# Kernel optimization log

Hardware: AMD Instinct MI355X
Metric: run time of the kernel (lower is better)

The kernel has to match this reference:

```python
import jax, jax.numpy as jnp
import numpy as np

N_NODES = 50000
N_EDGES = 800000
MUL = 32            # multiplicity of 0e and 1o feature irreps
N_SPECIES = 4       # node_attr = 4x0e one-hot
N_BASIS = 8         # radial basis scalars
N_HID = 8           # invariant_neurons
AVG_NEIGH = 16.0
INV_SQRT3 = 1.0 / np.sqrt(3.0).astype(np.float32)


def setup_inputs() -> dict:
    key = jax.random.key(0)
    ks = jax.random.split(key, 16)
    x = jax.random.normal(ks[0], (N_NODES, MUL * 4), jnp.float32)  # 32x0e + 32x1o
    species = jax.random.randint(ks[1], (N_NODES,), 0, N_SPECIES)
    node_attr = jax.nn.one_hot(species, N_SPECIES, dtype=jnp.float32)
    edge_embedding = jax.random.normal(ks[2], (N_EDGES, N_BASIS), jnp.float32)
    edge_attr = jax.random.normal(ks[3], (N_EDGES, 4), jnp.float32)  # 1x0e + 1x1o
    edge_index = jax.random.randint(ks[4], (2, N_EDGES), 0, N_NODES)
    # learned params
    W_lin1_s = jax.random.normal(ks[5], (MUL, MUL), jnp.float32)
    W_lin1_v = jax.random.normal(ks[6], (MUL, MUL), jnp.float32)
    fc_w1 = jax.random.normal(ks[7], (N_BASIS, N_HID), jnp.float32)
    fc_w2 = jax.random.normal(ks[8], (N_HID, 4 * MUL), jnp.float32)  # tp.weight_numel = 4*MUL
    W_lin2_s = jax.random.normal(ks[9], (2 * MUL, MUL), jnp.float32)  # mid simplify: 64x0e
    W_lin2_v = jax.random.normal(ks[10], (2 * MUL, MUL), jnp.float32)  # 64x1o
    W_sc_s = jax.random.normal(ks[11], (MUL, N_SPECIES, MUL), jnp.float32)
    W_sc_v = jax.random.normal(ks[12], (MUL, N_SPECIES, MUL), jnp.float32)
    return dict(node_features=x, node_attr=node_attr, edge_embedding=edge_embedding,
                edge_attr=edge_attr, edge_index=edge_index,
                W_lin1_s=W_lin1_s, W_lin1_v=W_lin1_v, fc_w1=fc_w1, fc_w2=fc_w2,
                W_lin2_s=W_lin2_s, W_lin2_v=W_lin2_v, W_sc_s=W_sc_s, W_sc_v=W_sc_v)


def _forward(node_features, node_attr, edge_embedding, edge_attr, edge_index,
             W_lin1_s, W_lin1_v, fc_w1, fc_w2, W_lin2_s, W_lin2_v, W_sc_s, W_sc_v):
    n = node_features.shape[0]
    xs = node_features[:, :MUL]                       # [N, 32] scalars (0e)
    xv = node_features[:, MUL:].reshape(n, MUL, 3)    # [N, 32, 3] vectors (1o)

    # self-connection: FullyConnectedTensorProduct(feat, 4x0e -> feat), uvw weights
    sc_norm = 1.0 / np.sqrt(MUL * N_SPECIES).astype(np.float32)
    sc_s = jnp.einsum('nu,nv,uvw->nw', xs, node_attr, W_sc_s) * sc_norm
    sc_v = jnp.einsum('nui,nv,uvw->nwi', xv, node_attr, W_sc_v) * sc_norm

    # linear_1: per-irrep channel mixing, 1/sqrt(fan_in)
    l1n = 1.0 / np.sqrt(MUL).astype(np.float32)
    ys = (xs @ W_lin1_s) * l1n
    yv = jnp.einsum('nui,uw->nwi', xv, W_lin1_v) * l1n

    # radial MLP -> per-edge tensor-product weights (4 paths x MUL)
    h = jax.nn.silu((edge_embedding @ fc_w1) / np.sqrt(N_BASIS).astype(np.float32))
    w = (h @ fc_w2) / np.sqrt(N_HID).astype(np.float32)  # [E, 128]
    w00, w01, w10, w11 = jnp.split(w, 4, axis=1)          # instruction order (0,0),(0,1),(1,0),(1,1)

    src = edge_index[0]
    dst = edge_index[1]
    es = ys[src]                                          # [E, 32]
    ev = yv[src]                                          # [E, 32, 3]
    a0 = edge_attr[:, 0]                                  # [E]    0e
    a1 = edge_attr[:, 1:4]                                # [E, 3] 1o

    # per-edge weighted uvu tensor product paths
    o_s_a = w00 * es * a0[:, None]                                       # 0e x 0e -> 0e
    o_s_b = w11 * jnp.einsum('eui,ei->eu', ev, a1) * INV_SQRT3           # 1o x 1o -> 0e
    o_v_a = (w01 * es)[:, :, None] * a1[:, None, :]                      # 0e x 1o -> 1o
    o_v_b = w10[:, :, None] * ev * a0[:, None, None]                     # 1o x 0e -> 1o

    # scatter-sum to destination nodes
    mid_s = jax.ops.segment_sum(jnp.concatenate([o_s_a, o_s_b], axis=1), dst, num_segments=n)
    mid_v = jax.ops.segment_sum(jnp.concatenate([o_v_a, o_v_b], axis=1), dst, num_segments=n)
    inv = 1.0 / np.sqrt(AVG_NEIGH).astype(np.float32)
    mid_s = mid_s * inv   # [N, 64]
    mid_v = mid_v * inv   # [N, 64, 3]

    # linear_2: 64x0e+64x1o -> 32x0e+32x1o
    l2n = 1.0 / np.sqrt(2 * MUL).astype(np.float32)
    out_s = (mid_s @ W_lin2_s) * l2n + sc_s
    out_v = jnp.einsum('nui,uw->nwi', mid_v, W_lin2_v) * l2n + sc_v
    return jnp.concatenate([out_s, out_v.reshape(n, MUL * 3)], axis=1)


def reference(node_features, node_attr, edge_embedding, edge_attr, edge_index,
              W_lin1_s, W_lin1_v, fc_w1, fc_w2, W_lin2_s, W_lin2_v, W_sc_s, W_sc_v):
    return _forward(node_features, node_attr, edge_embedding, edge_attr, edge_index,
                    W_lin1_s, W_lin1_v, fc_w1, fc_w2, W_lin2_s, W_lin2_v, W_sc_s, W_sc_v)
```

## Files before the change

kernel.cpp:

```cpp
#include <hip/hip_runtime.h>
#include <hip/hip_bf16.h>

#define N_NODES 50000
#define N_EDGES 800000
#define CAP 64

__global__ __launch_bounds__(256) void node_kernel(
    const float* __restrict__ x, const float* __restrict__ attr,
    const float* __restrict__ W1s, const float* __restrict__ W1v,
    const float* __restrict__ Wscs, const float* __restrict__ Wscv,
    float* __restrict__ ysv, float* __restrict__ out)
{
    __shared__ float lx[8][128];
    const int tid = threadIdx.x;
    const int node0 = blockIdx.x * 8;

    ((float4*)lx)[tid] = ((const float4*)(x + (long)node0 * 128))[tid];
    __syncthreads();

    const int nl = tid >> 5;
    const int w  = tid & 31;
    const int node = node0 + nl;

    const float* at = attr + (long)node * 4;
    int sp = 0;
    if (at[1] > 0.5f) sp = 1;
    if (at[2] > 0.5f) sp = 2;
    if (at[3] > 0.5f) sp = 3;

    float ys = 0.f, yv0 = 0.f, yv1 = 0.f, yv2 = 0.f;
    float ss = 0.f, sv0 = 0.f, sv1 = 0.f, sv2 = 0.f;
    #pragma unroll 8
    for (int u = 0; u < 32; ++u) {
        const float xs = lx[nl][u];
        const float x0 = lx[nl][32 + 3*u + 0];
        const float x1 = lx[nl][32 + 3*u + 1];
        const float x2 = lx[nl][32 + 3*u + 2];
        const float w1s = W1s[u*32 + w];
        const float w1v = W1v[u*32 + w];
        const float wss = Wscs[(u*4 + sp)*32 + w];
        const float wsv = Wscv[(u*4 + sp)*32 + w];
        ys  += xs * w1s;
        yv0 += x0 * w1v;  yv1 += x1 * w1v;  yv2 += x2 * w1v;
        ss  += xs * wss;
        sv0 += x0 * wsv;  sv1 += x1 * wsv;  sv2 += x2 * wsv;
    }
    const float l1n = 0.17677669529663687f;
    const float scn = 0.08838834764831843f;

    float* yp = ysv + (long)node * 128;
    yp[w]      = ys  * l1n;
    yp[32 + w] = yv0 * l1n;
    yp[64 + w] = yv1 * l1n;
    yp[96 + w] = yv2 * l1n;

    float* op = out + (long)node * 128;
    op[w] = ss * scn;
    op[32 + 3*w + 0] = sv0 * scn;
    op[32 + 3*w + 1] = sv1 * scn;
    op[32 + 3*w + 2] = sv2 * scn;
}

__global__ __launch_bounds__(256) void film_bucket_kernel(
    const float* __restrict__ ee, const float* __restrict__ eattr,
    const int* __restrict__ eidx, const float* __restrict__ fcw1,
    int* __restrict__ counts, int2* __restrict__ bucket,
    float* __restrict__ rec)
{
    __shared__ float fc1[64];
    const int tid = threadIdx.x;
    if (tid < 64) fc1[tid] = fcw1[tid];
    __syncthreads();

    const int e = blockIdx.x * 256 + tid;
    if (e < N_EDGES) {
        const float4 ea = ((const float4*)(ee + (long)e * 8))[0];
        const float4 eb = ((const float4*)(ee + (long)e * 8))[1];
        const float eev[8] = {ea.x, ea.y, ea.z, ea.w, eb.x, eb.y, eb.z, eb.w};
        const float inv_sqrt8 = 0.35355339059327373f;
        float h[8];
        #pragma unroll
        for (int j = 0; j < 8; ++j) {
            float pre = 0.f;
            #pragma unroll
            for (int b = 0; b < 8; ++b) pre += eev[b] * fc1[b*8 + j];
            pre *= inv_sqrt8;
            h[j] = pre / (1.f + __expf(-pre)) * inv_sqrt8;
        }
        float* rp = rec + (long)e * 12;
        ((float4*)rp)[0] = make_float4(h[0], h[1], h[2], h[3]);
        ((float4*)rp)[1] = make_float4(h[4], h[5], h[6], h[7]);
        ((float4*)rp)[2] = ((const float4*)eattr)[e];

        const int src = eidx[e];
        const int dst = eidx[N_EDGES + e];
        const int slot = atomicAdd(&counts[dst], 1);
        if (slot < CAP) bucket[(long)dst * CAP + slot] = make_int2(e, src);
    } else if (e == N_EDGES) {
        float* rp = rec + (long)e * 12;
        ((float4*)rp)[0] = make_float4(0.f, 0.f, 0.f, 0.f);
        ((float4*)rp)[1] = make_float4(0.f, 0.f, 0.f, 0.f);
        ((float4*)rp)[2] = make_float4(0.f, 0.f, 0.f, 0.f);
    }
}

__global__ __launch_bounds__(256) void agg_kernel(
    const float* __restrict__ fcw2,
    const float* __restrict__ W2s, const float* __restrict__ W2v,
    const float* __restrict__ ysv,
    const int* __restrict__ counts, const int2* __restrict__ bucket,
    const float* __restrict__ rec,
    float* __restrict__ out)
{
    __shared__ float w2s[2048];
    __shared__ float w2v[2048];
    __shared__ float mid[8][256];

    const int tid = threadIdx.x;
    for (int i = tid; i < 2048; i += 256) { w2s[i] = W2s[i]; w2v[i] = W2v[i]; }

    const int nl = tid >> 5;
    const int u  = tid & 31;
    const int node = blockIdx.x * 8 + nl;

    float f2r[8][4];
    #pragma unroll
    for (int j = 0; j < 8; ++j) {
        f2r[j][0] = fcw2[j*128 + u];
        f2r[j][1] = fcw2[j*128 + 32 + u];
        f2r[j][2] = fcw2[j*128 + 64 + u];
        f2r[j][3] = fcw2[j*128 + 96 + u];
    }

    const int cnt = min(counts[node], CAP);
    int2 b0 = bucket[(long)node * CAP + u];
    int2 b1 = bucket[(long)node * CAP + 32 + u];
    if (u >= cnt)      b0 = make_int2(N_EDGES, 0);
    if (32 + u >= cnt) b1 = make_int2(N_EDGES, 0);

    float msa = 0.f, msb = 0.f;
    float va0 = 0.f, va1 = 0.f, va2 = 0.f;
    float vb0 = 0.f, vb1 = 0.f, vb2 = 0.f;

    #define EDGE_PAIR(E0, S0, E1, S1)                                        \
    {                                                                        \
        const float4* r0 = (const float4*)(rec + (long)(E0) * 12);           \
        const float4* r1 = (const float4*)(rec + (long)(E1) * 12);           \
        const float4 h0a = r0[0], h0b = r0[1], at0 = r0[2];                  \
        const float4 h1a = r1[0], h1b = r1[1], at1 = r1[2];                  \
        const float* yp0 = ysv + (long)(S0) * 128;                           \
        const float* yp1 = ysv + (long)(S1) * 128;                           \
        const float es0 = yp0[u], ex0 = yp0[32+u], ey0 = yp0[64+u], ez0 = yp0[96+u]; \
        const float es1 = yp1[u], ex1 = yp1[32+u], ey1 = yp1[64+u], ez1 = yp1[96+u]; \
        const float h0[8] = {h0a.x,h0a.y,h0a.z,h0a.w,h0b.x,h0b.y,h0b.z,h0b.w}; \
        const float h1[8] = {h1a.x,h1a.y,h1a.z,h1a.w,h1b.x,h1b.y,h1b.z,h1b.w}; \
        float w00a=0.f,w01a=0.f,w10a=0.f,w11a=0.f;                           \
        float w00b=0.f,w01b=0.f,w10b=0.f,w11b=0.f;                           \
        _Pragma("unroll")                                                    \
        for (int j = 0; j < 8; ++j) {                                        \
            w00a += h0[j]*f2r[j][0]; w01a += h0[j]*f2r[j][1];                \
            w10a += h0[j]*f2r[j][2]; w11a += h0[j]*f2r[j][3];                \
            w00b += h1[j]*f2r[j][0]; w01b += h1[j]*f2r[j][1];                \
            w10b += h1[j]*f2r[j][2]; w11b += h1[j]*f2r[j][3];                \
        }                                                                    \
        {                                                                    \
            const float a0 = at0.x, a1x = at0.y, a1y = at0.z, a1z = at0.w;   \
            const float evdot = ex0*a1x + ey0*a1y + ez0*a1z;                 \
            msa += w00a * es0 * a0;                                          \
            msb += w11a * evdot;                                             \
            const float t = w01a * es0;                                      \
            va0 += t*a1x; va1 += t*a1y; va2 += t*a1z;                        \
            const float s = w10a * a0;                                       \
            vb0 += s*ex0; vb1 += s*ey0; vb2 += s*ez0;                        \
        }                                                                    \
        {                                                                    \
            const float a0 = at1.x, a1x = at1.y, a1y = at1.z, a1z = at1.w;   \
            const float evdot = ex1*a1x + ey1*a1y + ez1*a1z;                 \
            msa += w00b * es1 * a0;                                          \
            msb += w11b * evdot;                                             \
            const float t = w01b * es1;                                      \
            va0 += t*a1x; va1 += t*a1y; va2 += t*a1z;                        \
            const float s = w10b * a0;                                       \
            vb0 += s*ex1; vb1 += s*ey1; vb2 += s*ez1;                        \
        }                                                                    \
    }

    const int c0 = min(cnt, 32);
    for (int k = 0; k < c0; k += 2) {
        const int e0 = __shfl(b0.x, k, 32);
        const int s0 = __shfl(b0.y, k, 32);
        const int e1 = __shfl(b0.x, k + 1, 32);
        const int s1 = __shfl(b0.y, k + 1, 32);
        EDGE_PAIR(e0, s0, e1, s1)
    }
    if (cnt > 32) {
        for (int k = 32; k < cnt; k += 2) {
            const int e0 = __shfl(b1.x, k - 32, 32);
            const int s0 = __shfl(b1.y, k - 32, 32);
            const int e1 = __shfl(b1.x, k - 31, 32);
            const int s1 = __shfl(b1.y, k - 31, 32);
            EDGE_PAIR(e0, s0, e1, s1)
        }
    }
    #undef EDGE_PAIR

    msb *= 0.5773502691896258f;

    float* m = mid[nl];
    m[u]       = msa;
    m[32 + u]  = msb;
    m[64  + u*3 + 0] = va0;  m[64  + u*3 + 1] = va1;  m[64  + u*3 + 2] = va2;
    m[160 + u*3 + 0] = vb0;  m[160 + u*3 + 1] = vb1;  m[160 + u*3 + 2] = vb2;
    __syncthreads();

    float os = 0.f, ov0 = 0.f, ov1 = 0.f, ov2 = 0.f;
    #pragma unroll 8
    for (int q = 0; q < 32; ++q) {
        const float wsa = w2s[q*32 + u];
        const float wsb = w2s[(32 + q)*32 + u];
        os += m[q] * wsa + m[32 + q] * wsb;
        const float wva = w2v[q*32 + u];
        const float wvb = w2v[(32 + q)*32 + u];
        ov0 += m[64 + q*3 + 0] * wva + m[160 + q*3 + 0] * wvb;
        ov1 += m[64 + q*3 + 1] * wva + m[160 + q*3 + 1] * wvb;
        ov2 += m[64 + q*3 + 2] * wva + m[160 + q*3 + 2] * wvb;
    }

    const float sc = 0.03125f;
    float* op = out + (long)node * 128;
    op[u]            += os  * sc;
    op[32 + 3*u + 0] += ov0 * sc;
    op[32 + 3*u + 1] += ov1 * sc;
    op[32 + 3*u + 2] += ov2 * sc;
}

extern "C" void kernel_launch(void* const* d_in, const int* in_sizes, int n_in,
                              void* d_out, int out_size, void* d_ws, size_t ws_size,
                              hipStream_t stream) {
    const float* x     = (const float*)d_in[0];
    const float* attr  = (const float*)d_in[1];
    const float* ee    = (const float*)d_in[2];
    const float* eattr = (const float*)d_in[3];
    const int*   eidx  = (const int*)  d_in[4];
    const float* W1s   = (const float*)d_in[5];
    const float* W1v   = (const float*)d_in[6];
    const float* fcw1  = (const float*)d_in[7];
    const float* fcw2  = (const float*)d_in[8];
    const float* W2s   = (const float*)d_in[9];
    const float* W2v   = (const float*)d_in[10];
    const float* Wscs  = (const float*)d_in[11];
    const float* Wscv  = (const float*)d_in[12];

    float* out = (float*)d_out;

    float* ysv    = (float*)d_ws;
    int*   counts = (int*)(ysv + (long)N_NODES * 128);
    int2*  bucket = (int2*)(counts + N_NODES);
    float* rec    = (float*)(bucket + (long)N_NODES*CAP);

    hipMemsetAsync(counts, 0, N_NODES * sizeof(int), stream);
    node_kernel<<<N_NODES/8, 256, 0, stream>>>(x, attr, W1s, W1v, Wscs, Wscv, ysv, out);
    film_bucket_kernel<<<(N_EDGES + 256)/256, 256, 0, stream>>>(ee, eattr, eidx, fcw1,
                                                                counts, bucket, rec);
    agg_kernel<<<N_NODES/8, 256, 0, stream>>>(fcw2, W2s, W2v, ysv, counts, bucket, rec, out);
}
```

Baseline: 336.7 us.

## Merge node and edge prep kernels, store lin1 output in bf16, unroll gather by four

Fuses the node linear kernel and the edge FiLM/bucketing kernel into one launch, with block ranges split by blockIdx. The lin1 node features gathered per edge are stored in bf16 to halve gather traffic. The aggregation loop now processes four edges per iteration for more memory-level parallelism, and the second bucket half is loaded only when needed. Storing in bf16 reduces precision of the gathered features, and the 4-wide unroll relies on padding entries that point at a zero record.

```diff
diff --git a/kernel.cpp b/kernel.cpp
--- a/kernel.cpp
+++ b/kernel.cpp
@@ -4,110 +4,119 @@
 #define N_NODES 50000
 #define N_EDGES 800000
 #define CAP 64
-
-__global__ __launch_bounds__(256) void node_kernel(
+#define NODE_BLOCKS (N_NODES / 8)
+#define FILM_BLOCKS ((N_EDGES + 256) / 256)
+
+__device__ __forceinline__ float bf2f(unsigned short v) {
+    union { unsigned u; float f; } t; t.u = ((unsigned)v) << 16; return t.f;
+}
+__device__ __forceinline__ unsigned short f2bf(float f) {
+    union { float f; unsigned u; } t; t.f = f;
+    unsigned r = t.u + 0x7FFF + ((t.u >> 16) & 1);
+    return (unsigned short)(r >> 16);
+}
+
+__global__ __launch_bounds__(256) void prep_kernel(
     const float* __restrict__ x, const float* __restrict__ attr,
     const float* __restrict__ W1s, const float* __restrict__ W1v,
     const float* __restrict__ Wscs, const float* __restrict__ Wscv,
-    float* __restrict__ ysv, float* __restrict__ out)
-{
-    __shared__ float lx[8][128];
-    const int tid = threadIdx.x;
-    const int node0 = blockIdx.x * 8;
-
-    ((float4*)lx)[tid] = ((const float4*)(x + (long)node0 * 128))[tid];
-    __syncthreads();
-
-    const int nl = tid >> 5;
-    const int w  = tid & 31;
-    const int node = node0 + nl;
-
-    const float* at = attr + (long)node * 4;
-    int sp = 0;
-    if (at[1] > 0.5f) sp = 1;
-    if (at[2] > 0.5f) sp = 2;
-    if (at[3] > 0.5f) sp = 3;
-
-    float ys = 0.f, yv0 = 0.f, yv1 = 0.f, yv2 = 0.f;
-    float ss = 0.f, sv0 = 0.f, sv1 = 0.f, sv2 = 0.f;
-    #pragma unroll 8
-    for (int u = 0; u < 32; ++u) {
-        const float xs = lx[nl][u];
-        const float x0 = lx[nl][32 + 3*u + 0];
-        const float x1 = lx[nl][32 + 3*u + 1];
-        const float x2 = lx[nl][32 + 3*u + 2];
-        const float w1s = W1s[u*32 + w];
-        const float w1v = W1v[u*32 + w];
-        const float wss = Wscs[(u*4 + sp)*32 + w];
-        const float wsv = Wscv[(u*4 + sp)*32 + w];
-        ys  += xs * w1s;
-        yv0 += x0 * w1v;  yv1 += x1 * w1v;  yv2 += x2 * w1v;
-        ss  += xs * wss;
-        sv0 += x0 * wsv;  sv1 += x1 * wsv;  sv2 += x2 * wsv;
-    }
-    const float l1n = 0.17677669529663687f;
-    const float scn = 0.08838834764831843f;
-
-    float* yp = ysv + (long)node * 128;
-    yp[w]      = ys  * l1n;
-    yp[32 + w] = yv0 * l1n;
-    yp[64 + w] = yv1 * l1n;
-    yp[96 + w] = yv2 * l1n;
-
-    float* op = out + (long)node * 128;
-    op[w] = ss * scn;
-    op[32 + 3*w + 0] = sv0 * scn;
-    op[32 + 3*w + 1] = sv1 * scn;
-    op[32 + 3*w + 2] = sv2 * scn;
-}
-
-__global__ __launch_bounds__(256) void film_bucket_kernel(
     const float* __restrict__ ee, const float* __restrict__ eattr,
     const int* __restrict__ eidx, const float* __restrict__ fcw1,
     int* __restrict__ counts, int2* __restrict__ bucket,
-    float* __restrict__ rec)
+    float* __restrict__ rec,
+    unsigned short* __restrict__ ysvh, float* __restrict__ out)
 {
-    __shared__ float fc1[64];
+    __shared__ float shm[8 * 128];
     const int tid = threadIdx.x;
-    if (tid < 64) fc1[tid] = fcw1[tid];
-    __syncthreads();
-
-    const int e = blockIdx.x * 256 + tid;
-    if (e < N_EDGES) {
-        const float4 ea = ((const float4*)(ee + (long)e * 8))[0];
-        const float4 eb = ((const float4*)(ee + (long)e * 8))[1];
-        const float eev[8] = {ea.x, ea.y, ea.z, ea.w, eb.x, eb.y, eb.z, eb.w};
-        const float inv_sqrt8 = 0.35355339059327373f;
-        float h[8];
-        #pragma unroll
-        for (int j = 0; j < 8; ++j) {
-            float pre = 0.f;
+
+    if (blockIdx.x < NODE_BLOCKS) {
+        const int node0 = blockIdx.x * 8;
+        ((float4*)shm)[tid] = ((const float4*)(x + (long)node0 * 128))[tid];
+        __syncthreads();
+
+        const int nl = tid >> 5;
+        const int w  = tid & 31;
+        const int node = node0 + nl;
+
+        const float* at = attr + (long)node * 4;
+        int sp = 0;
+        if (at[1] > 0.5f) sp = 1;
+        if (at[2] > 0.5f) sp = 2;
+        if (at[3] > 0.5f) sp = 3;
+
+        const float* lx = shm + nl * 128;
+        float ys = 0.f, yv0 = 0.f, yv1 = 0.f, yv2 = 0.f;
+        float ss = 0.f, sv0 = 0.f, sv1 = 0.f, sv2 = 0.f;
+        #pragma unroll 8
+        for (int u = 0; u < 32; ++u) {
+            const float xs = lx[u];
+            const float x0 = lx[32 + 3*u + 0];
+            const float x1 = lx[32 + 3*u + 1];
+            const float x2 = lx[32 + 3*u + 2];
+            const float w1s = W1s[u*32 + w];
+            const float w1v = W1v[u*32 + w];
+            const float wss = Wscs[(u*4 + sp)*32 + w];
+            const float wsv = Wscv[(u*4 + sp)*32 + w];
+            ys  += xs * w1s;
+            yv0 += x0 * w1v;  yv1 += x1 * w1v;  yv2 += x2 * w1v;
+            ss  += xs * wss;
+            sv0 += x0 * wsv;  sv1 += x1 * wsv;  sv2 += x2 * wsv;
+        }
+        const float l1n = 0.17677669529663687f;
+        const float scn = 0.08838834764831843f;
+
+        unsigned short* yp = ysvh + (long)node * 128;
+        yp[w]      = f2bf(ys  * l1n);
+        yp[32 + w] = f2bf(yv0 * l1n);
+        yp[64 + w] = f2bf(yv1 * l1n);
+        yp[96 + w] = f2bf(yv2 * l1n);
+
+        float* op = out + (long)node * 128;
+        op[w] = ss * scn;
+        op[32 + 3*w + 0] = sv0 * scn;
+        op[32 + 3*w + 1] = sv1 * scn;
+        op[32 + 3*w + 2] = sv2 * scn;
+    } else {
+        if (tid < 64) shm[tid] = fcw1[tid];
+        __syncthreads();
+
+        const int e = (blockIdx.x - NODE_BLOCKS) * 256 + tid;
+        if (e < N_EDGES) {
+            const float4 ea = ((const float4*)(ee + (long)e * 8))[0];
+            const float4 eb = ((const float4*)(ee + (long)e * 8))[1];
+            const float eev[8] = {ea.x, ea.y, ea.z, ea.w, eb.x, eb.y, eb.z, eb.w};
+            const float inv_sqrt8 = 0.35355339059327373f;
+            float h[8];
             #pragma unroll
-            for (int b = 0; b < 8; ++b) pre += eev[b] * fc1[b*8 + j];
-            pre *= inv_sqrt8;
-            h[j] = pre / (1.f + __expf(-pre)) * inv_sqrt8;
+            for (int j = 0; j < 8; ++j) {
+                float pre = 0.f;
+                #pragma unroll
+                for (int b = 0; b < 8; ++b) pre += eev[b] * shm[b*8 + j];
+                pre *= inv_sqrt8;
+                h[j] = pre / (1.f + __expf(-pre)) * inv_sqrt8;
+            }
+            float* rp = rec + (long)e * 12;
+            ((float4*)rp)[0] = make_float4(h[0], h[1], h[2], h[3]);
+            ((float4*)rp)[1] = make_float4(h[4], h[5], h[6], h[7]);
+            ((float4*)rp)[2] = ((const float4*)eattr)[e];
+
+            const int src = eidx[e];
+            const int dst = eidx[N_EDGES + e];
+            const int slot = atomicAdd(&counts[dst], 1);
+            if (slot < CAP) bucket[(long)dst * CAP + slot] = make_int2(e, src);
+        } else if (e == N_EDGES) {
+            float* rp = rec + (long)e * 12;
+            ((float4*)rp)[0] = make_float4(0.f, 0.f, 0.f, 0.f);
+            ((float4*)rp)[1] = make_float4(0.f, 0.f, 0.f, 0.f);
+            ((float4*)rp)[2] = make_float4(0.f, 0.f, 0.f, 0.f);
         }
-        float* rp = rec + (long)e * 12;
-        ((float4*)rp)[0] = make_float4(h[0], h[1], h[2], h[3]);
-        ((float4*)rp)[1] = make_float4(h[4], h[5], h[6], h[7]);
-        ((float4*)rp)[2] = ((const float4*)eattr)[e];
-
-        const int src = eidx[e];
-        const int dst = eidx[N_EDGES + e];
-        const int slot = atomicAdd(&counts[dst], 1);
-        if (slot < CAP) bucket[(long)dst * CAP + slot] = make_int2(e, src);
-    } else if (e == N_EDGES) {
-        float* rp = rec + (long)e * 12;
-        ((float4*)rp)[0] = make_float4(0.f, 0.f, 0.f, 0.f);
-        ((float4*)rp)[1] = make_float4(0.f, 0.f, 0.f, 0.f);
-        ((float4*)rp)[2] = make_float4(0.f, 0.f, 0.f, 0.f);
     }
 }
 
 __global__ __launch_bounds__(256) void agg_kernel(
     const float* __restrict__ fcw2,
     const float* __restrict__ W2s, const float* __restrict__ W2v,
-    const float* __restrict__ ysv,
+    const unsigned short* __restrict__ ysvh,
     const int* __restrict__ counts, const int2* __restrict__ bucket,
     const float* __restrict__ rec,
     float* __restrict__ out)
@@ -134,75 +143,69 @@
 
     const int cnt = min(counts[node], CAP);
     int2 b0 = bucket[(long)node * CAP + u];
-    int2 b1 = bucket[(long)node * CAP + 32 + u];
-    if (u >= cnt)      b0 = make_int2(N_EDGES, 0);
-    if (32 + u >= cnt) b1 = make_int2(N_EDGES, 0);
+    if (u >= cnt) b0 = make_int2(N_EDGES, 0);
 
     float msa = 0.f, msb = 0.f;
     float va0 = 0.f, va1 = 0.f, va2 = 0.f;
     float vb0 = 0.f, vb1 = 0.f, vb2 = 0.f;
 
-    #define EDGE_PAIR(E0, S0, E1, S1)                                        \
+    #define ACCUM(HA, HB, AT, US, UX, UY, UZ)                                \
     {                                                                        \
-        const float4* r0 = (const float4*)(rec + (long)(E0) * 12);           \
-        const float4* r1 = (const float4*)(rec + (long)(E1) * 12);           \
-        const float4 h0a = r0[0], h0b = r0[1], at0 = r0[2];                  \
-        const float4 h1a = r1[0], h1b = r1[1], at1 = r1[2];                  \
-        const float* yp0 = ysv + (long)(S0) * 128;                           \
-        const float* yp1 = ysv + (long)(S1) * 128;                           \
-        const float es0 = yp0[u], ex0 = yp0[32+u], ey0 = yp0[64+u], ez0 = yp0[96+u]; \
-        const float es1 = yp1[u], ex1 = yp1[32+u], ey1 = yp1[64+u], ez1 = yp1[96+u]; \
-        const float h0[8] = {h0a.x,h0a.y,h0a.z,h0a.w,h0b.x,h0b.y,h0b.z,h0b.w}; \
-        const float h1[8] = {h1a.x,h1a.y,h1a.z,h1a.w,h1b.x,h1b.y,h1b.z,h1b.w}; \
-        float w00a=0.f,w01a=0.f,w10a=0.f,w11a=0.f;                           \
-        float w00b=0.f,w01b=0.f,w10b=0.f,w11b=0.f;                           \
+        const float es = bf2f(US), ex = bf2f(UX), ey = bf2f(UY), ez = bf2f(UZ); \
+        const float hh[8] = {HA.x,HA.y,HA.z,HA.w,HB.x,HB.y,HB.z,HB.w};       \
+        float w00=0.f, w01=0.f, w10=0.f, w11=0.f;                            \
         _Pragma("unroll")                                                    \
         for (int j = 0; j < 8; ++j) {                                        \
-            w00a += h0[j]*f2r[j][0]; w01a += h0[j]*f2r[j][1];                \
-            w10a += h0[j]*f2r[j][2]; w11a += h0[j]*f2r[j][3];                \
-            w00b += h1[j]*f2r[j][0]; w01b += h1[j]*f2r[j][1];                \
-            w10b += h1[j]*f2r[j][2]; w11b += h1[j]*f2r[j][3];                \
+            w00 += hh[j]*f2r[j][0]; w01 += hh[j]*f2r[j][1];                  \
+            w10 += hh[j]*f2r[j][2]; w11 += hh[j]*f2r[j][3];                  \
         }                                                                    \
-        {                                                                    \
-            const float a0 = at0.x, a1x = at0.y, a1y = at0.z, a1z = at0.w;   \
-            const float evdot = ex0*a1x + ey0*a1y + ez0*a1z;                 \
-            msa += w00a * es0 * a0;                                          \
-            msb += w11a * evdot;                                             \
-            const float t = w01a * es0;                                      \
-            va0 += t*a1x; va1 += t*a1y; va2 += t*a1z;                        \
-            const float s = w10a * a0;                                       \
-            vb0 += s*ex0; vb1 += s*ey0; vb2 += s*ez0;                        \
-        }                                                                    \
-        {                                                                    \
-            const float a0 = at1.x, a1x = at1.y, a1y = at1.z, a1z = at1.w;   \
-            const float evdot = ex1*a1x + ey1*a1y + ez1*a1z;                 \
-            msa += w00b * es1 * a0;                                          \
-            msb += w11b * evdot;                                             \
-            const float t = w01b * es1;                                      \
-            va0 += t*a1x; va1 += t*a1y; va2 += t*a1z;                        \
-            const float s = w10b * a0;                                       \
-            vb0 += s*ex1; vb1 += s*ey1; vb2 += s*ez1;                        \
-        }                                                                    \
+        const float a0 = AT.x, a1x = AT.y, a1y = AT.z, a1z = AT.w;           \
+        msa += w00 * es * a0;                                                \
+        msb += w11 * (ex*a1x + ey*a1y + ez*a1z);                             \
+        const float t = w01 * es;                                            \
+        va0 += t*a1x; va1 += t*a1y; va2 += t*a1z;                            \
+        const float s = w10 * a0;                                            \
+        vb0 += s*ex; vb1 += s*ey; vb2 += s*ez;                               \
+    }
+
+    #define QUAD(BX, BY, KOFF)                                               \
+    {                                                                        \
+        const int e0 = __shfl(BX, (KOFF)+0, 32), s0 = __shfl(BY, (KOFF)+0, 32); \
+        const int e1 = __shfl(BX, (KOFF)+1, 32), s1 = __shfl(BY, (KOFF)+1, 32); \
+        const int e2 = __shfl(BX, (KOFF)+2, 32), s2 = __shfl(BY, (KOFF)+2, 32); \
+        const int e3 = __shfl(BX, (KOFF)+3, 32), s3 = __shfl(BY, (KOFF)+3, 32); \
+        const float4* r0 = (const float4*)(rec + (long)e0 * 12);             \
+        const float4* r1 = (const float4*)(rec + (long)e1 * 12);             \
+        const float4* r2 = (const float4*)(rec + (long)e2 * 12);             \
+        const float4* r3 = (const float4*)(rec + (long)e3 * 12);             \
+        const unsigned short* y0 = ysvh + (long)s0 * 128;                    \
+        const unsigned short* y1 = ysvh + (long)s1 * 128;                    \
+        const unsigned short* y2 = ysvh + (long)s2 * 128;                    \
+        const unsigned short* y3 = ysvh + (long)s3 * 128;                    \
+        const float4 h0a = r0[0], h0b = r0[1], t0 = r0[2];                   \
+        const float4 h1a = r1[0], h1b = r1[1], t1 = r1[2];                   \
+        const float4 h2a = r2[0], h2b = r2[1], t2 = r2[2];                   \
+        const float4 h3a = r3[0], h3b = r3[1], t3 = r3[2];                   \
+        const unsigned short us0=y0[u], ux0=y0[32+u], uy0=y0[64+u], uz0=y0[96+u]; \
+        const unsigned short us1=y1[u], ux1=y1[32+u], uy1=y1[64+u], uz1=y1[96+u]; \
+        const unsigned short us2=y2[u], ux2=y2[32+u], uy2=y2[64+u], uz2=y2[96+u]; \
+        const unsigned short us3=y3[u], ux3=y3[32+u], uy3=y3[64+u], uz3=y3[96+u]; \
+        ACCUM(h0a, h0b, t0, us0, ux0, uy0, uz0)                              \
+        ACCUM(h1a, h1b, t1, us1, ux1, uy1, uz1)                              \
+        ACCUM(h2a, h2b, t2, us2, ux2, uy2, uz2)                              \
+        ACCUM(h3a, h3b, t3, us3, ux3, uy3, uz3)                              \
     }
 
     const int c0 = min(cnt, 32);
-    for (int k = 0; k < c0; k += 2) {
-        const int e0 = __shfl(b0.x, k, 32);
-        const int s0 = __shfl(b0.y, k, 32);
-        const int e1 = __shfl(b0.x, k + 1, 32);
-        const int s1 = __shfl(b0.y, k + 1, 32);
-        EDGE_PAIR(e0, s0, e1, s1)
-    }
+    for (int k = 0; k < c0; k += 4) QUAD(b0.x, b0.y, k)
+
     if (cnt > 32) {
-        for (int k = 32; k < cnt; k += 2) {
-            const int e0 = __shfl(b1.x, k - 32, 32);
-            const int s0 = __shfl(b1.y, k - 32, 32);
-            const int e1 = __shfl(b1.x, k - 31, 32);
-            const int s1 = __shfl(b1.y, k - 31, 32);
-            EDGE_PAIR(e0, s0, e1, s1)
-        }
-    }
-    #undef EDGE_PAIR
+        int2 b1 = bucket[(long)node * CAP + 32 + u];
+        if (32 + u >= cnt) b1 = make_int2(N_EDGES, 0);
+        for (int k = 0; k < cnt - 32; k += 4) QUAD(b1.x, b1.y, k)
+    }
+    #undef QUAD
+    #undef ACCUM
 
     msb *= 0.5773502691896258f;
 
@@ -253,14 +256,15 @@
 
     float* out = (float*)d_out;
 
-    float* ysv    = (float*)d_ws;
-    int*   counts = (int*)(ysv + (long)N_NODES * 128);
+    unsigned short* ysvh = (unsigned short*)d_ws;
+    int*   counts = (int*)(ysvh + (long)N_NODES * 128);
     int2*  bucket = (int2*)(counts + N_NODES);
-    float* rec    = (float*)(bucket + (long)N_NODES*CAP);
+    float* rec    = (float*)(bucket + (long)N_NODES * CAP);
 
     hipMemsetAsync(counts, 0, N_NODES * sizeof(int), stream);
-    node_kernel<<<N_NODES/8, 256, 0, stream>>>(x, attr, W1s, W1v, Wscs, Wscv, ysv, out);
-    film_bucket_kernel<<<(N_EDGES + 256)/256, 256, 0, stream>>>(ee, eattr, eidx, fcw1,
-                                                                counts, bucket, rec);
-    agg_kernel<<<N_NODES/8, 256, 0, stream>>>(fcw2, W2s, W2v, ysv, counts, bucket, rec, out);
-}
+    prep_kernel<<<NODE_BLOCKS + FILM_BLOCKS, 256, 0, stream>>>(
+        x, attr, W1s, W1v, Wscs, Wscv, ee, eattr, eidx, fcw1,
+        counts, bucket, rec, ysvh, out);
+    agg_kernel<<<N_NODES/8, 256, 0, stream>>>(fcw2, W2s, W2v, ysvh,
+                                              counts, bucket, rec, out);
+}
```

After: 439.0 us. 30.4% more time.
